# Performance work log

Hardware: AMD Instinct MI355X
Metric: run time of the kernel (lower is better)

## Reference

```python
import jax, jax.numpy as jnp
import numpy as np

N = 51200      # num nodes
E = 614400     # num edges
G = 256        # num graphs
T = 8          # num target capsules (GCNConv heads)
D = 128        # in_channels == out_channels
ROUTES = 3     # num_routes
BN_EPS = 1e-5


def squash(s):
    # s: (..., D). v = |s|^2/(1+|s|^2) * s/|s|
    s2 = jnp.sum(s * s, axis=-1, keepdims=True)
    return (s2 / (1.0 + s2)) * s * jax.lax.rsqrt(s2 + 1e-16)


def setup_inputs() -> dict:
    key = jax.random.key(0)
    k0, k1, k2, k3 = jax.random.split(key, 4)
    x = jax.random.normal(k0, (N, D), dtype=jnp.float32)
    edge_index = jax.random.randint(k1, (2, E), 0, N, dtype=jnp.int32)
    batch = jnp.sort(jax.random.randint(k2, (N,), 0, G, dtype=jnp.int32))
    edge_weight = jnp.ones((E,), dtype=jnp.float32)
    gamma = jnp.ones((D,), dtype=jnp.float32)
    beta = jnp.zeros((D,), dtype=jnp.float32)
    W = jax.random.normal(k3, (T, D, D), dtype=jnp.float32) * (1.0 / np.sqrt(D))
    bias = jnp.zeros((T, D), dtype=jnp.float32)
    return {"x": x, "edge_weight": edge_weight, "gamma": gamma, "beta": beta,
            "W": W, "bias": bias, "edge_index": edge_index, "batch": batch}


def reference(x, edge_weight, gamma, beta, W, bias, edge_index, batch):
    n = x.shape[0]
    row, col = edge_index[0], edge_index[1]

    # BatchNorm1d (training-mode batch stats)
    mu = jnp.mean(x, axis=0)
    var = jnp.var(x, axis=0)
    x = (x - mu) * jax.lax.rsqrt(var + BN_EPS) * gamma + beta

    # --- GCNConv per target capsule (PyG gcn_norm with self-loops) ---
    sl = jnp.arange(n, dtype=row.dtype)
    row_sl = jnp.concatenate([row, sl])
    col_sl = jnp.concatenate([col, sl])
    w_sl = jnp.concatenate([edge_weight, jnp.ones((n,), x.dtype)])
    deg = jax.ops.segment_sum(w_sl, col_sl, num_segments=n)
    dis = jnp.where(deg > 0, jax.lax.rsqrt(jnp.maximum(deg, 1e-12)), 0.0)
    norm = dis[row_sl] * w_sl * dis[col_sl]          # (E+N,)

    xW = jnp.einsum('nd,tdo->nto', x, W)             # (N, T, D)
    caps = []
    for t in range(T):  # small fixed loop over capsule heads keeps edge msgs at (E+N, D)
        msg = norm[:, None] * xW[row_sl, t]          # (E+N, D)
        caps.append(jax.ops.segment_sum(msg, col_sl, num_segments=n) + bias[t])
    u_hat = jnp.stack(caps, axis=1)                  # (N, T, D)

    # --- dynamic routing ---
    node_deg = jax.ops.segment_sum(edge_weight, row, num_segments=n)  # original edges, no self loops
    b = jnp.broadcast_to(node_deg[:, None, None], (n, T, 1))
    u_det = jax.lax.stop_gradient(u_hat)
    for _ in range(ROUTES - 1):
        c = jax.nn.softmax(b, axis=1)                               # (N, T, 1)
        s = jax.ops.segment_sum(c * u_det, batch, num_segments=G)   # (G, T, D)
        v = squash(s)[batch]                                        # (N, T, D)
        b = b + jnp.sum(u_det * v, axis=-1, keepdims=True)

    c = jax.nn.softmax(b, axis=1)
    s = jax.ops.segment_sum(c * u_hat, batch, num_segments=G)        # (G, T, D)
    cnt = jax.ops.segment_sum(jnp.ones((n,), x.dtype), batch, num_segments=G)
    x_mean = jax.ops.segment_sum(x, batch, num_segments=G) / jnp.maximum(cnt, 1.0)[:, None]
    s = s + x_mean[:, None, :]
    v = squash(s)
    # final_layer=True: per-capsule L2 norm -> (G, T)
    return jnp.sqrt(jnp.sum(v * v, axis=-1) + 1e-16)
```

## Files before the change

kernel.cpp:

```cpp
#include <hip/hip_runtime.h>
#include <hip/hip_bf16.h>
#include <math.h>

#define N_NODES 51200
#define N_EDGES 614400
#define N_GRAPHS 256
#define T_CAPS 8
#define D_DIM 128
#define BN_EPS 1e-5f
#define RCAP 256
#define NBUCK 200
#define BCAP 4096
#define EPB 1024
#define SBLK 600

typedef __attribute__((ext_vector_type(8))) __bf16 bf16x8;
typedef __attribute__((ext_vector_type(8))) unsigned short ushort8;
typedef __attribute__((ext_vector_type(4))) float f32x4;

__device__ inline f32x4 mfma16(uint4 a, uint4 b, f32x4 c) {
  return __builtin_amdgcn_mfma_f32_16x16x32_bf16(
      __builtin_bit_cast(bf16x8, a), __builtin_bit_cast(bf16x8, b), c, 0, 0, 0);
}
__device__ inline f32x4 mfma16v(uint4 a, ushort8 b, f32x4 c) {
  return __builtin_amdgcn_mfma_f32_16x16x32_bf16(
      __builtin_bit_cast(bf16x8, a), __builtin_bit_cast(bf16x8, b), c, 0, 0, 0);
}

__device__ inline float waveReduceSum(float v) {
#pragma unroll
  for (int off = 1; off < 64; off <<= 1) v += __shfl_xor(v, off, 64);
  return v;
}
__device__ inline float bf_lo(unsigned u) { return __uint_as_float(u << 16); }
__device__ inline float bf_hi(unsigned u) { return __uint_as_float(u & 0xffff0000u); }
__device__ inline unsigned bfbits(float f) {
  unsigned u = __float_as_uint(f);
  return (u + 0x7FFFu + ((u >> 16) & 1u)) >> 16;
}

__global__ void __launch_bounds__(256) prep(const int* __restrict__ batch,
                                            const float* __restrict__ W,
                                            int* __restrict__ start, int* __restrict__ bcur,
                                            unsigned* __restrict__ Wfrag,
                                            unsigned* __restrict__ WTfrag,
                                            float* __restrict__ rawzero) {
  int i = blockIdx.x * 256 + threadIdx.x;
  if (i < NBUCK) bcur[i] = 0;
  for (int j = i; j < 2 * N_GRAPHS * D_DIM; j += N_NODES) rawzero[j] = 0.f;
  int bn = batch[i];
  if (i == 0) {
    for (int g = 0; g <= bn; g++) start[g] = 0;
  } else {
    int bp = batch[i - 1];
    for (int g = bp + 1; g <= bn; g++) start[g] = i;
  }
  if (i == N_NODES - 1)
    for (int g = bn + 1; g <= N_GRAPHS; g++) start[g] = N_NODES;
  for (int dd = i; dd < 65536; dd += N_NODES) {
    int jj = dd & 3, lane = (dd >> 2) & 63, ks = (dd >> 8) & 3;
    int nt = (dd >> 10) & 7, t = dd >> 13;
    int k = ks * 32 + ((lane >> 4) << 3) + 2 * jj;
    int n = nt * 16 + (lane & 15);
    float a = W[(t << 14) + (k << 7) + n];
    float b = W[(t << 14) + ((k + 1) << 7) + n];
    Wfrag[dd] = bfbits(a) | (bfbits(b) << 16);
    float2 w2 = ((const float2*)W)[((t << 14) + (n << 7) + k) >> 1];
    WTfrag[dd] = bfbits(w2.x) | (bfbits(w2.y) << 16);
  }
}

__global__ void __launch_bounds__(256) scatter_x(
    const int* __restrict__ row, const int* __restrict__ col, const float* __restrict__ ew,
    int* __restrict__ bcur, uint2* __restrict__ ebuck, const float* __restrict__ x,
    const int* __restrict__ start, float* __restrict__ rawxsum, float* __restrict__ rawxsq) {
  int bid = blockIdx.x, tid = threadIdx.x;
  if (bid < SBLK) {
    __shared__ uint2 staged[EPB];
    __shared__ int hcnt[256], lbase[256], gbase[256], wpart[4];
    unsigned rx[4], ry[4];
    int bk[4], idx[4];
    int base4 = bid * 256 + tid;
    int4 c4 = ((const int4*)col)[base4];
    int4 r4 = ((const int4*)row)[base4];
    float4 w4 = ((const float4*)ew)[base4];
    rx[0] = ((unsigned)c4.x << 16) | (unsigned)r4.x; ry[0] = bfbits(w4.x); bk[0] = c4.x >> 8;
    rx[1] = ((unsigned)c4.y << 16) | (unsigned)r4.y; ry[1] = bfbits(w4.y); bk[1] = c4.y >> 8;
    rx[2] = ((unsigned)c4.z << 16) | (unsigned)r4.z; ry[2] = bfbits(w4.z); bk[2] = c4.z >> 8;
    rx[3] = ((unsigned)c4.w << 16) | (unsigned)r4.w; ry[3] = bfbits(w4.w); bk[3] = c4.w >> 8;
    hcnt[tid] = 0;
    __syncthreads();
#pragma unroll
    for (int k = 0; k < 4; k++) idx[k] = atomicAdd(&hcnt[bk[k]], 1);
    __syncthreads();
    int v = hcnt[tid];
    int lane = tid & 63, wid = tid >> 6;
    int s = v;
#pragma unroll
    for (int off = 1; off < 64; off <<= 1) {
      int t = __shfl_up(s, off, 64);
      if (lane >= off) s += t;
    }
    if (lane == 63) wpart[wid] = s;
    if (tid < NBUCK) gbase[tid] = atomicAdd(&bcur[tid], v);
    __syncthreads();
    int add = 0;
    for (int w2 = 0; w2 < wid; w2++) add += wpart[w2];
    lbase[tid] = s + add - v;
    __syncthreads();
#pragma unroll
    for (int k = 0; k < 4; k++) staged[lbase[bk[k]] + idx[k]] = make_uint2(rx[k], ry[k]);
    __syncthreads();
    for (int i = tid; i < EPB; i += 256) {
      uint2 r = staged[i];
      int b = r.x >> 24;
      int pos = gbase[b] + (i - lbase[b]);
      if (pos < BCAP) ebuck[b * BCAP + pos] = r;
    }
    return;
  }
  int b2 = bid - SBLK;
  int g = b2 >> 2, sub = b2 & 3;
  __shared__ float ls[8][128], ls2[8][128];
  int q = tid & 31, h = tid >> 5;
  int st = start[g], en = start[g + 1];
  const float4* x4 = (const float4*)x;
  float4 s = make_float4(0.f, 0.f, 0.f, 0.f), s2 = make_float4(0.f, 0.f, 0.f, 0.f);
  for (int n = st + sub * 8 + h; n < en; n += 32) {
    float4 v = x4[n * 32 + q];
    s.x += v.x; s.y += v.y; s.z += v.z; s.w += v.w;
    s2.x += v.x * v.x; s2.y += v.y * v.y; s2.z += v.z * v.z; s2.w += v.w * v.w;
  }
  *(float4*)&ls[h][4 * q] = s;
  *(float4*)&ls2[h][4 * q] = s2;
  __syncthreads();
  if (tid < 128) {
    float a = 0.f;
#pragma unroll
    for (int hh = 0; hh < 8; hh++) a += ls[hh][tid];
    atomicAdd(&rawxsum[g * D_DIM + tid], a);
  } else {
    int d = tid - 128;
    float a = 0.f;
#pragma unroll
    for (int hh = 0; hh < 8; hh++) a += ls2[hh][d];
    atomicAdd(&rawxsq[g * D_DIM + d], a);
  }
}

__global__ void __launch_bounds__(256) bn_fin(const float* __restrict__ rawxsum,
                                              const float* __restrict__ rawxsq,
                                              const float* __restrict__ gamma,
                                              const float* __restrict__ beta,
                                              float* __restrict__ scale,
                                              float* __restrict__ shift) {
  int d = blockIdx.x;
  int tid = threadIdx.x;
  __shared__ float ls[256], ls2[256];
  ls[tid] = rawxsum[tid * D_DIM + d];
  ls2[tid] = rawxsq[tid * D_DIM + d];
  __syncthreads();
  for (int off = 128; off; off >>= 1) {
    if (tid < off) {
      ls[tid] += ls[tid + off];
      ls2[tid] += ls2[tid + off];
    }
    __syncthreads();
  }
  if (tid == 0) {
    float mu = ls[0] * (1.0f / N_NODES);
    float var = ls2[0] * (1.0f / N_NODES) - mu * mu;
    float rstd = rsqrtf(var + BN_EPS);
    float sc = gamma[d] * rstd;
    scale[d] = sc;
    shift[d] = beta[d] - mu * sc;
  }
}

__global__ void __launch_bounds__(256) build(const uint2* __restrict__ ebuck,
                                             const int* __restrict__ bcur,
                                             unsigned* __restrict__ csr,
                                             int* __restrict__ nstart, int* __restrict__ ncnt,
                                             const float* __restrict__ x,
                                             const float* __restrict__ scale,
                                             const float* __restrict__ shift,
                                             float* __restrict__ dis,
                                             __hip_bfloat162* __restrict__ y) {
  int b = blockIdx.x, tid = threadIdx.x;
  __shared__ uint2 staged[BCAP];
  __shared__ unsigned outr[BCAP];
  __shared__ int hist[256], pref[256], cur[256], wpart[4];
  __shared__ float dis_l[256];
  int cnt = min(bcur[b], BCAP);
  for (int i = tid; i < cnt; i += 256) staged[i] = ebuck[b * BCAP + i];
  hist[tid] = 0;
  __syncthreads();
  for (int i = tid; i < cnt; i += 256) {
    int dl = (staged[i].x >> 16) & 255;
    atomicAdd(&hist[dl], 1);
  }
  __syncthreads();
  int v = hist[tid];
  int lane = tid & 63, wid = tid >> 6;
  int s = v;
#pragma unroll
  for (int off = 1; off < 64; off <<= 1) {
    int t = __shfl_up(s, off, 64);
    if (lane >= off) s += t;
  }
  if (lane == 63) wpart[wid] = s;
  __syncthreads();
  int add = 0;
  for (int w2 = 0; w2 < wid; w2++) add += wpart[w2];
  int p0 = s + add - v;
  pref[tid] = p0;
  cur[tid] = p0;
  __syncthreads();
  for (int i = tid; i < cnt; i += 256) {
    uint2 r = staged[i];
    int dl = (r.x >> 16) & 255;
    int p = atomicAdd(&cur[dl], 1);
    outr[p] = ((r.x & 0xFFFFu) << 16) | r.y;
  }
  __syncthreads();
  for (int i = tid; i < cnt; i += 256) csr[b * BCAP + i] = outr[i];
  int n = b * 256 + tid;
  int hc = hist[tid];
  nstart[n] = b * BCAP + p0;
  ncnt[n] = hc;
  float sw = 0.f;
  for (int j = p0; j < p0 + hc; j++) sw += bf_lo(outr[j]);
  float dv = sw + 1.0f;
  float dn = dv > 0.f ? rsqrtf(fmaxf(dv, 1e-12f)) : 0.f;
  dis[n] = dn;
  dis_l[tid] = dn;
  __syncthreads();
  const float4* x4 = (const float4*)x;
  const float4* sc4 = (const float4*)scale;
  const float4* sh4 = (const float4*)shift;
  uint2* y2 = (uint2*)y;
  for (int i = tid; i < 256 * 32; i += 256) {
    int nl = i >> 5, l = i & 31;
    float dnl = dis_l[nl];
    float4 scv = sc4[l], shv = sh4[l];
    float4 xv = x4[(b * 256 + nl) * 32 + l];
    unsigned u0 = bfbits(dnl * (xv.x * scv.x + shv.x)) |
                  (bfbits(dnl * (xv.y * scv.y + shv.y)) << 16);
    unsigned u1 = bfbits(dnl * (xv.z * scv.z + shv.z)) |
                  (bfbits(dnl * (xv.w * scv.w + shv.w)) << 16);
    y2[(b * 256 + nl) * 32 + l] = make_uint2(u0, u1);
  }
}

__global__ void __launch_bounds__(256) node_gather(const __hip_bfloat162* __restrict__ y,
                                                   const float* __restrict__ dis,
                                                   const int* __restrict__ nstart,
                                                   const int* __restrict__ ncnt,
                                                   const unsigned* __restrict__ csr,
                                                   __hip_bfloat162* __restrict__ agg) {
  int n = blockIdx.x * 4 + (threadIdx.x >> 6);
  int lane = threadIdx.x & 63;
  int st = nstart[n], c = ncnt[n];
  float2 a = __bfloat1622float2(y[n * 64 + lane]);
  int j = 0;
  for (; j + 4 <= c; j += 4) {
    unsigned r0 = csr[st + j], r1 = csr[st + j + 1], r2 = csr[st + j + 2],
             r3 = csr[st + j + 3];
    float2 v0 = __bfloat1622float2(y[(r0 >> 16) * 64 + lane]);
    float2 v1 = __bfloat1622float2(y[(r1 >> 16) * 64 + lane]);
    float2 v2 = __bfloat1622float2(y[(r2 >> 16) * 64 + lane]);
    float2 v3 = __bfloat1622float2(y[(r3 >> 16) * 64 + lane]);
    float w0 = bf_lo(r0), w1 = bf_lo(r1), w2 = bf_lo(r2), w3 = bf_lo(r3);
    a.x += w0 * v0.x + w1 * v1.x + w2 * v2.x + w3 * v3.x;
    a.y += w0 * v0.y + w1 * v1.y + w2 * v2.y + w3 * v3.y;
  }
  for (; j < c; j++) {
    unsigned r = csr[st + j];
    float2 v = __bfloat1622float2(y[(r >> 16) * 64 + lane]);
    float w = bf_lo(r);
    a.x += w * v.x;
    a.y += w * v.y;
  }
  float dn = dis[n];
  a.x *= dn;
  a.y *= dn;
  agg[n * 64 + lane] = __float22bfloat162_rn(a);
}

__global__ void __launch_bounds__(1024, 4) routing_fused(
    const unsigned* __restrict__ agg_bf, const int* __restrict__ start,
    const unsigned* __restrict__ Wfrag, const unsigned* __restrict__ WTfrag,
    const float* __restrict__ bias, const float* __restrict__ rawxsum,
    const float* __restrict__ scale, const float* __restrict__ shift,
    float* __restrict__ out) {
  int g = blockIdx.x;
  int tid = threadIdx.x;
  int st = start[g], c = start[g + 1] - st;

  __shared__ unsigned ag_sh[RCAP * 68];
  __shared__ float dt_sh[384][T_CAPS];
  __shared__ float ac_sh[T_CAPS][D_DIM];
  __shared__ float s_sh[T_CAPS][D_DIM];
  __shared__ float wv_sh[T_CAPS][132];
  __shared__ unsigned wvpk[2][16][68];
  __shared__ unsigned short ctb[2][16][264];
  __shared__ unsigned acpk[T_CAPS][2][64];
  __shared__ unsigned spk[T_CAPS][2][64];
  __shared__ float csum_sh[T_CAPS], bv_sh[T_CAPS], f_sh[T_CAPS], s2p[T_CAPS][2];
  __shared__ float csp_sh[32];

  float* scratch = &dt_sh[0][0];
  const uint4* aggb4 = (const uint4*)agg_bf;
  uint4* ag4 = (uint4*)ag_sh;

  for (int i = tid; i < T_CAPS * 132; i += 1024) (&wv_sh[0][0])[i] = 0.f;
  for (int i = tid; i < 2 * 16 * 68; i += 1024) (&wvpk[0][0][0])[i] = 0u;
  for (int i = tid; i < 2 * 16 * 264; i += 1024) (&ctb[0][0][0])[i] = 0;
  if (tid < T_CAPS) {
    bv_sh[tid] = 0.f;
    csum_sh[tid] = 0.125f * (float)c;
  }
  {
    int d2 = tid & 63, h = tid >> 6;
    float sx = 0.f, sy = 0.f;
    for (int n = st + h; n < st + c; n += 16) {
      unsigned u = agg_bf[n * 64 + d2];
      sx += bf_lo(u);
      sy += bf_hi(u);
    }
    scratch[h * 128 + d2 * 2] = sx;
    scratch[h * 128 + d2 * 2 + 1] = sy;
  }
  __syncthreads();
  if (tid < 128) {
    float s = 0.f;
#pragma unroll
    for (int h = 0; h < 16; h++) s += scratch[h * 128 + tid];
    s *= 0.125f;
#pragma unroll
    for (int t = 0; t < T_CAPS; t++) ac_sh[t][tid] = s;
  }
  __syncthreads();

  int tG = tid >> 7, oG = tid & 127;
  int lane = tid & 63, wv_ = tid >> 6;

  for (int iter = 0; iter < 3; iter++) {
    {
      int t = tid >> 7, m = (tid >> 6) & 1, kp = tid & 63;
      float a = ac_sh[t][2 * kp], b = ac_sh[t][2 * kp + 1];
      unsigned ha = bfbits(a), hb = bfbits(b);
      if (m == 0)
        acpk[t][0][kp] = ha | (hb << 16);
      else
        acpk[t][1][kp] = bfbits(a - __uint_as_float(ha << 16)) |
                         (bfbits(b - __uint_as_float(hb << 16)) << 16);
    }
    __syncthreads();
    {
      int t = wv_ & 7, oh = wv_ >> 3;
      int m = lane & 15, q = lane >> 4;
      const uint4* Wf = (const uint4*)Wfrag;
#pragma unroll 1
      for (int cq = 0; cq < 4; cq++) {
        f32x4 C = {0.f, 0.f, 0.f, 0.f};
#pragma unroll
        for (int ks = 0; ks < 4; ks++) {
          uint4 A = (m < 2) ? *(const uint4*)&acpk[t][m][ks * 16 + q * 4]
                            : make_uint4(0, 0, 0, 0);
          uint4 B = Wf[((t * 8 + oh * 4 + cq) * 4 + ks) * 64 + lane];
          C = mfma16(A, B, C);
        }
        if (q == 0) s_sh[t][oh * 64 + cq * 16 + m] = C[0] + C[1];
      }
    }
    __syncthreads();
    {
      float s = s_sh[tG][oG] + csum_sh[tG] * bias[(tG << 7) + oG];
      if (iter == 2) {
        float cf = (float)c;
        float ic = 1.0f / fmaxf(cf, 1.0f);
        s += (scale[oG] * rawxsum[g * D_DIM + oG] + cf * shift[oG]) * ic;
      }
      s_sh[tG][oG] = s;
      float p = waveReduceSum(s * s);
      if ((tid & 63) == 0) s2p[tG][(tid >> 6) & 1] = p;
    }
    __syncthreads();
    {
      int t = tid >> 7, m = (tid >> 6) & 1, kp = tid & 63;
      float a = s_sh[t][2 * kp], b = s_sh[t][2 * kp + 1];
      unsigned ha = bfbits(a), hb = bfbits(b);
      if (m == 0)
        spk[t][0][kp] = ha | (hb << 16);
      else
        spk[t][1][kp] = bfbits(a - __uint_as_float(ha << 16)) |
                        (bfbits(b - __uint_as_float(hb << 16)) << 16);
    }
    if (tid < T_CAPS) {
      float s2 = s2p[tid][0] + s2p[tid][1];
      float f = (s2 / (1.0f + s2)) * rsqrtf(s2 + 1e-16f);
      f_sh[tid] = f;
      if (iter == 2) out[g * T_CAPS + tid] = sqrtf(f * f * s2 + 1e-16f);
    }
    __syncthreads();
    if (iter == 2) return;
    {
      int t = wv_ & 7, oh = wv_ >> 3;
      int m = lane & 15, q = lane >> 4;
      const uint4* Wf = (const uint4*)WTfrag;
#pragma unroll 1
      for (int cq = 0; cq < 4; cq++) {
        f32x4 C = {0.f, 0.f, 0.f, 0.f};
#pragma unroll
        for (int ks = 0; ks < 4; ks++) {
          uint4 A = (m < 2) ? *(const uint4*)&spk[t][m][ks * 16 + q * 4]
                            : make_uint4(0, 0, 0, 0);
          uint4 B = Wf[((t * 8 + oh * 4 + cq) * 4 + ks) * 64 + lane];
          C = mfma16(A, B, C);
        }
        if (q == 0) scratch[t * 128 + oh * 64 + cq * 16 + m] = C[0] + C[1];
      }
    }
    __syncthreads();
    {
      wv_sh[tG][oG] += f_sh[tG] * scratch[tG * 128 + oG];
      float bp = bias[(tG << 7) + oG] * s_sh[tG][oG];
      bp = waveReduceSum(bp);
      if ((tid & 63) == 0) s2p[tG][(tid >> 6) & 1] = bp;
    }
    __syncthreads();
    if (tid < T_CAPS) bv_sh[tid] += f_sh[tid] * (s2p[tid][0] + s2p[tid][1]);
    __syncthreads();
    for (int i = tid; i < 512; i += 1024) {
      int t = i >> 6, kp = i & 63;
      float a = wv_sh[t][2 * kp], b = wv_sh[t][2 * kp + 1];
      unsigned ha = bfbits(a), hb = bfbits(b);
      wvpk[0][t][kp] = ha | (hb << 16);
      float ra = a - __uint_as_float(ha << 16), rb = b - __uint_as_float(hb << 16);
      wvpk[1][t][kp] = bfbits(ra) | (bfbits(rb) << 16);
    }
    if (tid < 1024) {
      (&ac_sh[0][0])[tid] = 0.f;
    }
    if (tid < T_CAPS) csum_sh[tid] = 0.f;
    __syncthreads();

    for (int cb = 0; cb < c; cb += RCAP) {
      int nv = min(RCAP, c - cb);
      int KR32 = (nv + 31) & ~31;
      int Mt = (nv + 15) >> 4;
      if (iter == 0 || c > RCAP) {
        for (int i = tid; i < nv * 16; i += 1024) {
          int r = i >> 4, k = i & 15;
          ag4[r * 17 + k] = aggb4[(size_t)(st + cb + r) * 16 + k];
        }
        for (int i = tid; i < (KR32 - nv) * 16; i += 1024) {
          int r = nv + (i >> 4), k = i & 15;
          ag4[r * 17 + k] = make_uint4(0, 0, 0, 0);
        }
        __syncthreads();
      }
      if (wv_ < Mt) {
        int q = lane >> 4, tc = lane & 15;
        int r = wv_ * 16 + tc;
        const uint4* arow = ag4 + r * 17;
        f32x4 C = {0.f, 0.f, 0.f, 0.f};
#pragma unroll
        for (int ks = 0; ks < 4; ks++) {
          uint4 A = arow[ks * 4 + q];
          uint4 Bh = *(const uint4*)&wvpk[0][tc][ks * 16 + 4 * q];
          uint4 Bl = *(const uint4*)&wvpk[1][tc][ks * 16 + 4 * q];
          C = mfma16(A, Bh, C);
          C = mfma16(A, Bl, C);
        }
        if (tc < T_CAPS) {
          float bvv = bv_sh[tc];
#pragma unroll
          for (int i2 = 0; i2 < 4; i2++) dt_sh[wv_ * 16 + 4 * q + i2][tc] = C[i2] + bvv;
        }
      }
      __syncthreads();
      if (tid < nv) {
        float l[8];
#pragma unroll
        for (int t = 0; t < 8; t++) l[t] = dt_sh[tid][t];
        float m = l[0];
#pragma unroll
        for (int t = 1; t < 8; t++) m = fmaxf(m, l[t]);
        float z = 0.f;
#pragma unroll
        for (int t = 0; t < 8; t++) {
          l[t] = __expf(l[t] - m);
          z += l[t];
        }
        float iz = 1.0f / z;
#pragma unroll
        for (int t = 0; t < 8; t++) {
          float cv = l[t] * iz;
          dt_sh[tid][t] = cv;
          unsigned hb = bfbits(cv);
          ctb[0][t][tid] = (unsigned short)hb;
          ctb[1][t][tid] = (unsigned short)bfbits(cv - __uint_as_float(hb << 16));
        }
      }
      if (c > RCAP) {
        int tail = KR32 - nv;
        for (int i = tid; i < 16 * tail; i += 1024) {
          int hh = i & 1, t = (i >> 1) & 7, n2 = nv + (i >> 4);
          ctb[hh][t][n2] = 0;
        }
      }
      __syncthreads();
      {
        int tA = tid >> 7, idx = tid & 127;
        float p = 0.f;
        for (int n = idx; n < nv; n += 128) p += dt_sh[n][tA];
        p = waveReduceSum(p);
        if (lane == 0) csp_sh[wv_] = p;
      }
      __syncthreads();
      if (tid < T_CAPS) csum_sh[tid] += csp_sh[2 * tid] + csp_sh[2 * tid + 1];
      {
        int nt = wv_ & 7, kh = wv_ >> 3;
        int tc = lane & 15, q = lane >> 4;
        f32x4 C = {0.f, 0.f, 0.f, 0.f};
        const unsigned short* agh = (const unsigned short*)ag_sh;
        int KS = KR32 >> 5;
        for (int ks = kh; ks < KS; ks += 2) {
          uint4 Ah = *(const uint4*)&ctb[0][tc][ks * 32 + 8 * q];
          uint4 Al = *(const uint4*)&ctb[1][tc][ks * 32 + 8 * q];
          int nb = ks * 32 + 8 * q, dcol = nt * 16 + tc;
          ushort8 B;
#pragma unroll
          for (int j = 0; j < 8; j++) B[j] = agh[(nb + j) * 136 + dcol];
          C = mfma16v(Ah, B, C);
          C = mfma16v(Al, B, C);
        }
        if (kh == 1) *(f32x4*)&scratch[(nt * 64 + lane) * 4] = C;
        __syncthreads();
        if (kh == 0) {
          f32x4 o4 = *(const f32x4*)&scratch[(nt * 64 + lane) * 4];
          C.x += o4.x;
          C.y += o4.y;
          C.z += o4.z;
          C.w += o4.w;
#pragma unroll
          for (int i2 = 0; i2 < 4; i2++) {
            int tt = 4 * q + i2;
            if (tt < T_CAPS) ac_sh[tt][nt * 16 + tc] += C[i2];
          }
        }
      }
      __syncthreads();
    }
  }
}

extern "C" void kernel_launch(void* const* d_in, const int* in_sizes, int n_in, void* d_out,
                              int out_size, void* d_ws, size_t ws_size, hipStream_t stream) {
  const float* x = (const float*)d_in[0];
  const float* ew = (const float*)d_in[1];
  const float* gamma = (const float*)d_in[2];
  const float* beta = (const float*)d_in[3];
  const float* W = (const float*)d_in[4];
  const float* bias = (const float*)d_in[5];
  const int* eidx = (const int*)d_in[6];
  const int* batch = (const int*)d_in[7];
  float* out = (float*)d_out;
  float* w = (float*)d_ws;

  const int* row = eidx;
  const int* col = eidx + N_EDGES;

  int* bcur = (int*)w;
  int* start = bcur + 256;
  float* scale = (float*)(start + 260);
  float* shift = scale + 128;
  float* dis = shift + 128;
  float* rawxsum = dis + N_NODES;
  float* rawxsq = rawxsum + N_GRAPHS * D_DIM;
  unsigned* Wfrag = (unsigned*)(rawxsq + N_GRAPHS * D_DIM);
  unsigned* WTfrag = Wfrag + 65536;
  int* nstart = (int*)(WTfrag + 65536);
  int* ncnt = nstart + N_NODES;
  uint2* ebuck = (uint2*)(ncnt + N_NODES);
  unsigned* csr = (unsigned*)(ebuck + (size_t)NBUCK * BCAP);
  __hip_bfloat162* y = (__hip_bfloat162*)(csr + (size_t)NBUCK * BCAP);
  unsigned* agg_bf = (unsigned*)(y + (size_t)N_NODES * 64);

  prep<<<N_NODES / 256, 256, 0, stream>>>(batch, W, start, bcur, Wfrag, WTfrag, rawxsum);
  scatter_x<<<SBLK + 4 * N_GRAPHS, 256, 0, stream>>>(row, col, ew, bcur, ebuck, x, start,
                                                     rawxsum, rawxsq);
  bn_fin<<<D_DIM, 256, 0, stream>>>(rawxsum, rawxsq, gamma, beta, scale, shift);
  build<<<NBUCK, 256, 0, stream>>>(ebuck, bcur, csr, nstart, ncnt, x, scale, shift, dis, y);
  node_gather<<<N_NODES / 4, 256, 0, stream>>>(y, dis, nstart, ncnt, csr,
                                               (__hip_bfloat162*)agg_bf);
  routing_fused<<<N_GRAPHS, 1024, 0, stream>>>(agg_bf, start, Wfrag, WTfrag, bias, rawxsum,
                                               scale, shift, out);
}
```

Measured before the change: 190.8 us.

## Run BN finalize alongside CSR build and split y construction into its own kernel

Merges the batchnorm-finalize kernel and the per-bucket CSR build into one launch. Blocks 0-127 compute the scale and shift, and the remaining blocks, now 512 threads each, build the CSR and compute dis. The normalized y write moves into a separate, more parallel kernel with 800 blocks, so the CSR sort no longer waits on BN stats and y is no longer produced by only 200 blocks. The gather loop also gets an 8-way unrolled path to keep more loads in flight. The cost is an extra launch plus rereading dis and x from global memory.

Result: faster. 182.8 us (-4.2%).

```diff
diff --git a/kernel.cpp b/kernel.cpp
--- a/kernel.cpp
+++ b/kernel.cpp
@@ -148,59 +148,58 @@
   }
 }
 
-__global__ void __launch_bounds__(256) bn_fin(const float* __restrict__ rawxsum,
-                                              const float* __restrict__ rawxsq,
-                                              const float* __restrict__ gamma,
-                                              const float* __restrict__ beta,
-                                              float* __restrict__ scale,
-                                              float* __restrict__ shift) {
-  int d = blockIdx.x;
-  int tid = threadIdx.x;
-  __shared__ float ls[256], ls2[256];
-  ls[tid] = rawxsum[tid * D_DIM + d];
-  ls2[tid] = rawxsq[tid * D_DIM + d];
-  __syncthreads();
-  for (int off = 128; off; off >>= 1) {
-    if (tid < off) {
-      ls[tid] += ls[tid + off];
-      ls2[tid] += ls2[tid + off];
-    }
-    __syncthreads();
-  }
-  if (tid == 0) {
-    float mu = ls[0] * (1.0f / N_NODES);
-    float var = ls2[0] * (1.0f / N_NODES) - mu * mu;
-    float rstd = rsqrtf(var + BN_EPS);
-    float sc = gamma[d] * rstd;
-    scale[d] = sc;
-    shift[d] = beta[d] - mu * sc;
-  }
-}
-
-__global__ void __launch_bounds__(256) build(const uint2* __restrict__ ebuck,
-                                             const int* __restrict__ bcur,
-                                             unsigned* __restrict__ csr,
-                                             int* __restrict__ nstart, int* __restrict__ ncnt,
-                                             const float* __restrict__ x,
-                                             const float* __restrict__ scale,
-                                             const float* __restrict__ shift,
-                                             float* __restrict__ dis,
-                                             __hip_bfloat162* __restrict__ y) {
-  int b = blockIdx.x, tid = threadIdx.x;
+__global__ void __launch_bounds__(512) mid(const float* __restrict__ rawxsum,
+                                           const float* __restrict__ rawxsq,
+                                           const float* __restrict__ gamma,
+                                           const float* __restrict__ beta,
+                                           float* __restrict__ scale,
+                                           float* __restrict__ shift,
+                                           const uint2* __restrict__ ebuck,
+                                           const int* __restrict__ bcur,
+                                           unsigned* __restrict__ csr,
+                                           int* __restrict__ nstart, int* __restrict__ ncnt,
+                                           float* __restrict__ dis) {
+  int bid = blockIdx.x, tid = threadIdx.x;
   __shared__ uint2 staged[BCAP];
   __shared__ unsigned outr[BCAP];
-  __shared__ int hist[256], pref[256], cur[256], wpart[4];
-  __shared__ float dis_l[256];
+  __shared__ int hist[256], pref[256], cur[256], wpart[8];
+  if (bid < 128) {
+    int d = bid;
+    float* ls = (float*)staged;
+    float* ls2 = ls + 256;
+    if (tid < 256) {
+      ls[tid] = rawxsum[tid * D_DIM + d];
+      ls2[tid] = rawxsq[tid * D_DIM + d];
+    }
+    __syncthreads();
+    for (int off = 128; off; off >>= 1) {
+      if (tid < off) {
+        ls[tid] += ls[tid + off];
+        ls2[tid] += ls2[tid + off];
+      }
+      __syncthreads();
+    }
+    if (tid == 0) {
+      float mu = ls[0] * (1.0f / N_NODES);
+      float var = ls2[0] * (1.0f / N_NODES) - mu * mu;
+      float rstd = rsqrtf(var + BN_EPS);
+      float sc = gamma[d] * rstd;
+      scale[d] = sc;
+      shift[d] = beta[d] - mu * sc;
+    }
+    return;
+  }
+  int b = bid - 128;
   int cnt = min(bcur[b], BCAP);
-  for (int i = tid; i < cnt; i += 256) staged[i] = ebuck[b * BCAP + i];
-  hist[tid] = 0;
-  __syncthreads();
-  for (int i = tid; i < cnt; i += 256) {
+  for (int i = tid; i < cnt; i += 512) staged[i] = ebuck[b * BCAP + i];
+  if (tid < 256) hist[tid] = 0;
+  __syncthreads();
+  for (int i = tid; i < cnt; i += 512) {
     int dl = (staged[i].x >> 16) & 255;
     atomicAdd(&hist[dl], 1);
   }
   __syncthreads();
-  int v = hist[tid];
+  int v = (tid < 256) ? hist[tid] : 0;
   int lane = tid & 63, wid = tid >> 6;
   int s = v;
 #pragma unroll
@@ -208,47 +207,58 @@
     int t = __shfl_up(s, off, 64);
     if (lane >= off) s += t;
   }
-  if (lane == 63) wpart[wid] = s;
-  __syncthreads();
-  int add = 0;
-  for (int w2 = 0; w2 < wid; w2++) add += wpart[w2];
-  int p0 = s + add - v;
-  pref[tid] = p0;
-  cur[tid] = p0;
-  __syncthreads();
-  for (int i = tid; i < cnt; i += 256) {
+  if (lane == 63 && wid < 4) wpart[wid] = s;
+  __syncthreads();
+  int p0 = 0;
+  if (tid < 256) {
+    int add = 0;
+    for (int w2 = 0; w2 < wid; w2++) add += wpart[w2];
+    p0 = s + add - v;
+    pref[tid] = p0;
+    cur[tid] = p0;
+  }
+  __syncthreads();
+  for (int i = tid; i < cnt; i += 512) {
     uint2 r = staged[i];
     int dl = (r.x >> 16) & 255;
     int p = atomicAdd(&cur[dl], 1);
     outr[p] = ((r.x & 0xFFFFu) << 16) | r.y;
   }
   __syncthreads();
-  for (int i = tid; i < cnt; i += 256) csr[b * BCAP + i] = outr[i];
-  int n = b * 256 + tid;
-  int hc = hist[tid];
-  nstart[n] = b * BCAP + p0;
-  ncnt[n] = hc;
-  float sw = 0.f;
-  for (int j = p0; j < p0 + hc; j++) sw += bf_lo(outr[j]);
-  float dv = sw + 1.0f;
-  float dn = dv > 0.f ? rsqrtf(fmaxf(dv, 1e-12f)) : 0.f;
-  dis[n] = dn;
-  dis_l[tid] = dn;
-  __syncthreads();
+  for (int i = tid; i < cnt; i += 512) csr[b * BCAP + i] = outr[i];
+  if (tid < 256) {
+    int n = b * 256 + tid;
+    int hc = hist[tid];
+    nstart[n] = b * BCAP + p0;
+    ncnt[n] = hc;
+    float sw = 0.f;
+    for (int j = p0; j < p0 + hc; j++) sw += bf_lo(outr[j]);
+    float dv = sw + 1.0f;
+    dis[n] = dv > 0.f ? rsqrtf(fmaxf(dv, 1e-12f)) : 0.f;
+  }
+}
+
+__global__ void __launch_bounds__(256) y_build(const float* __restrict__ x,
+                                               const float* __restrict__ scale,
+                                               const float* __restrict__ shift,
+                                               const float* __restrict__ dis,
+                                               __hip_bfloat162* __restrict__ y) {
+  int base = blockIdx.x * 64;
   const float4* x4 = (const float4*)x;
   const float4* sc4 = (const float4*)scale;
   const float4* sh4 = (const float4*)shift;
   uint2* y2 = (uint2*)y;
-  for (int i = tid; i < 256 * 32; i += 256) {
+  for (int i = threadIdx.x; i < 64 * 32; i += 256) {
     int nl = i >> 5, l = i & 31;
-    float dnl = dis_l[nl];
+    int n = base + nl;
+    float dnl = dis[n];
     float4 scv = sc4[l], shv = sh4[l];
-    float4 xv = x4[(b * 256 + nl) * 32 + l];
+    float4 xv = x4[n * 32 + l];
     unsigned u0 = bfbits(dnl * (xv.x * scv.x + shv.x)) |
                   (bfbits(dnl * (xv.y * scv.y + shv.y)) << 16);
     unsigned u1 = bfbits(dnl * (xv.z * scv.z + shv.z)) |
                   (bfbits(dnl * (xv.w * scv.w + shv.w)) << 16);
-    y2[(b * 256 + nl) * 32 + l] = make_uint2(u0, u1);
+    y2[n * 32 + l] = make_uint2(u0, u1);
   }
 }
 
@@ -263,6 +273,20 @@
   int st = nstart[n], c = ncnt[n];
   float2 a = __bfloat1622float2(y[n * 64 + lane]);
   int j = 0;
+  for (; j + 8 <= c; j += 8) {
+    unsigned r[8];
+#pragma unroll
+    for (int k = 0; k < 8; k++) r[k] = csr[st + j + k];
+    float2 v[8];
+#pragma unroll
+    for (int k = 0; k < 8; k++) v[k] = __bfloat1622float2(y[(r[k] >> 16) * 64 + lane]);
+#pragma unroll
+    for (int k = 0; k < 8; k++) {
+      float w = bf_lo(r[k]);
+      a.x += w * v[k].x;
+      a.y += w * v[k].y;
+    }
+  }
   for (; j + 4 <= c; j += 4) {
     unsigned r0 = csr[st + j], r1 = csr[st + j + 1], r2 = csr[st + j + 2],
              r3 = csr[st + j + 3];
@@ -592,8 +616,9 @@
   prep<<<N_NODES / 256, 256, 0, stream>>>(batch, W, start, bcur, Wfrag, WTfrag, rawxsum);
   scatter_x<<<SBLK + 4 * N_GRAPHS, 256, 0, stream>>>(row, col, ew, bcur, ebuck, x, start,
                                                      rawxsum, rawxsq);
-  bn_fin<<<D_DIM, 256, 0, stream>>>(rawxsum, rawxsq, gamma, beta, scale, shift);
-  build<<<NBUCK, 256, 0, stream>>>(ebuck, bcur, csr, nstart, ncnt, x, scale, shift, dis, y);
+  mid<<<128 + NBUCK, 512, 0, stream>>>(rawxsum, rawxsq, gamma, beta, scale, shift, ebuck,
+                                       bcur, csr, nstart, ncnt, dis);
+  y_build<<<N_NODES / 64, 256, 0, stream>>>(x, scale, shift, dis, y);
   node_gather<<<N_NODES / 4, 256, 0, stream>>>(y, dis, nstart, ncnt, csr,
                                                (__hip_bfloat162*)agg_bf);
   routing_fused<<<N_GRAPHS, 1024, 0, stream>>>(agg_bf, start, Wfrag, WTfrag, bias, rawxsum,
```
